# Kernel optimization log

Measured on AMD Instinct MI355X. Metric: run time of the kernel, lower is better.

The kernel has to match this reference:

```python
import math
import jax, jax.numpy as jnp
import numpy as np

B, L, D = 8, 512, 32
SEQ_LEN = 512.0
N_PATCHES, N_REF = 16, 32
LAT, HM = 128, 4
FH, NL, FF = 8, 3, 128
PRED = 96

def _time_embed(t, d):
    # interleaved sin/cos embedding, matching PositionalEmbedding's div_term
    div = jnp.exp(jnp.arange(0, d, 2, dtype=jnp.float32) * (-math.log(10000.0) / d))
    ang = t[..., None] * div
    out = jnp.zeros(t.shape + (d,), dtype=jnp.float32)
    return out.at[..., 0::2].set(jnp.sin(ang)).at[..., 1::2].set(jnp.cos(ang))

def _layernorm(x, g, b):
    mu = jnp.mean(x, axis=-1, keepdims=True)
    var = jnp.var(x, axis=-1, keepdims=True)
    return (x - mu) / jnp.sqrt(var + 1e-5) * g + b

def _mha(z, Wq, Wk, Wv, Wo, bq, bk, bv, bo):
    N, S, dm = z.shape
    hd = dm // FH
    q = (z @ Wq + bq).reshape(N, S, FH, hd)
    k = (z @ Wk + bk).reshape(N, S, FH, hd)
    v = (z @ Wv + bv).reshape(N, S, FH, hd)
    s = jnp.einsum('nqhe,nkhe->nhqk', q, k) / math.sqrt(hd)
    a = jax.nn.softmax(s, axis=-1)
    o = jnp.einsum('nhqk,nkhe->nqhe', a, v).reshape(N, S, dm)
    return o @ Wo + bo

def _forward(x, x_mark, x_mask, Wq, Wk, W_out, b_out, f_Wq, f_Wk, f_Wv, f_Wo, f_bq, f_bk, f_bv, f_bo, f_ln1_g, f_ln1_b, f_W1, f_b1, f_W2, f_b2, f_ln2_g, f_ln2_b, ln_f_g, ln_f_b, W_lin, b_lin):
    t = x_mark[:, :, 0]                                   # [B, L] irregular timestamps in [0, SEQ_LEN]
    edges = jnp.linspace(0.0, SEQ_LEN, N_PATCHES + 1)
    refs = jnp.linspace(0.0, SEQ_LEN, N_REF * N_PATCHES).reshape(N_PATCHES, N_REF)
    obs_valid = jnp.sum(x_mask, axis=-1) > 0              # [B, L]
    dk = LAT // HM
    Kmat = (_time_embed(t, LAT) @ Wk).reshape(B, L, HM, dk)
    v = x * x_mask                                        # mask values like `v = v * m` in original
    reprs = []
    for i in range(N_PATCHES):  # fixed small structural loop
        # _split_patch equivalent: per-channel masked attention is permutation
        # invariant, so the sort/scatter compaction reduces to masking.
        in_patch = (t >= edges[i]) & (t <= edges[i + 1]) & obs_valid   # [B, L]
        Qi = (_time_embed(refs[i], LAT) @ Wq).reshape(N_REF, HM, dk)
        scores = jnp.einsum('rhe,blhe->bhrl', Qi, Kmat) / math.sqrt(dk)
        cmask = x_mask * in_patch[..., None].astype(x.dtype)           # [B, L, D]
        neg = jnp.where(cmask[:, None, None, :, :] > 0, 0.0, -1e9)     # [B,1,1,L,D]
        p = jax.nn.softmax(scores[..., None] + neg, axis=3)            # [B,H,R,L,D]
        attn = jnp.einsum('bhrld,bld->brhd', p, v)                     # [B,R,H,D]
        reprs.append(attn.reshape(B, N_REF, HM * D) @ W_out + b_out)   # [B,R,D]
    rp = jnp.stack(reprs, axis=1)                          # [B, NP, R, D]
    z = rp.transpose(0, 3, 1, 2).reshape(B * D, N_PATCHES, N_REF)
    z = z + _time_embed(jnp.arange(N_PATCHES, dtype=jnp.float32), N_REF)[None]
    for l in range(NL):
        a = _mha(z, f_Wq[l], f_Wk[l], f_Wv[l], f_Wo[l], f_bq[l], f_bk[l], f_bv[l], f_bo[l])
        z = _layernorm(z + a, f_ln1_g[l], f_ln1_b[l])
        y = jax.nn.gelu(z @ f_W1[l] + f_b1[l]) @ f_W2[l] + f_b2[l]
        z = _layernorm(z + y, f_ln2_g[l], f_ln2_b[l])
    z = _layernorm(z, ln_f_g, ln_f_b)
    emb = z.reshape(B, D, N_PATCHES, N_REF).transpose(0, 1, 3, 2)      # [B, D, R, NP]
    out = emb.reshape(B, D, N_REF * N_PATCHES) @ W_lin + b_lin         # [B, D, PRED]
    return out.transpose(0, 2, 1)                          # [B, PRED, D]

def setup_inputs():
    key = jax.random.key(0)
    ks = jax.random.split(key, 30)
    def w(i, shape, fan_in):
        return jax.random.normal(ks[i], shape, jnp.float32) / math.sqrt(fan_in)
    return {
        'x': jax.random.normal(ks[0], (B, L, D), jnp.float32),
        'x_mark': jnp.sort(jax.random.uniform(ks[1], (B, L, 1), jnp.float32) * SEQ_LEN, axis=1),
        'x_mask': (jax.random.uniform(ks[2], (B, L, D), jnp.float32) < 0.8).astype(jnp.float32),
        'Wq': w(3, (LAT, LAT), LAT),
        'Wk': w(4, (LAT, LAT), LAT),
        'W_out': w(5, (HM * D, D), HM * D),
        'b_out': jnp.zeros((D,), jnp.float32),
        'f_Wq': w(6, (NL, N_REF, N_REF), N_REF),
        'f_Wk': w(7, (NL, N_REF, N_REF), N_REF),
        'f_Wv': w(8, (NL, N_REF, N_REF), N_REF),
        'f_Wo': w(9, (NL, N_REF, N_REF), N_REF),
        'f_bq': jnp.zeros((NL, N_REF), jnp.float32),
        'f_bk': jnp.zeros((NL, N_REF), jnp.float32),
        'f_bv': jnp.zeros((NL, N_REF), jnp.float32),
        'f_bo': jnp.zeros((NL, N_REF), jnp.float32),
        'f_ln1_g': jnp.ones((NL, N_REF), jnp.float32),
        'f_ln1_b': jnp.zeros((NL, N_REF), jnp.float32),
        'f_W1': w(10, (NL, N_REF, FF), N_REF),
        'f_b1': jnp.zeros((NL, FF), jnp.float32),
        'f_W2': w(11, (NL, FF, N_REF), FF),
        'f_b2': jnp.zeros((NL, N_REF), jnp.float32),
        'f_ln2_g': jnp.ones((NL, N_REF), jnp.float32),
        'f_ln2_b': jnp.zeros((NL, N_REF), jnp.float32),
        'ln_f_g': jnp.ones((N_REF,), jnp.float32),
        'ln_f_b': jnp.zeros((N_REF,), jnp.float32),
        'W_lin': w(12, (N_REF * N_PATCHES, PRED), N_REF * N_PATCHES),
        'b_lin': jnp.zeros((PRED,), jnp.float32),
    }

def reference(x, x_mark, x_mask, Wq, Wk, W_out, b_out, f_Wq, f_Wk, f_Wv, f_Wo, f_bq, f_bk, f_bv, f_bo, f_ln1_g, f_ln1_b, f_W1, f_b1, f_W2, f_b2, f_ln2_g, f_ln2_b, ln_f_g, ln_f_b, W_lin, b_lin):
    return _forward(x, x_mark, x_mask, Wq, Wk, W_out, b_out, f_Wq, f_Wk, f_Wv, f_Wo, f_bq, f_bk, f_bv, f_bo, f_ln1_g, f_ln1_b, f_W1, f_b1, f_W2, f_b2, f_ln2_g, f_ln2_b, ln_f_g, ln_f_b, W_lin, b_lin)
```

## Files before the change

kernel.cpp:

```cpp
#include <hip/hip_runtime.h>
#include <math.h>


#define ISQ32 0.17677669529663687f
#define C128  (-0.07195578415606394f)
#define C32   (-0.28782313662425575f)

__launch_bounds__(256)
__global__ void k_embed_mm(const float* __restrict__ x_mark,
                           const float* __restrict__ Wk,
                           const float* __restrict__ Wq,
                           const float* __restrict__ x_mask,
                           float* __restrict__ Kmat,
                           float* __restrict__ Qall,
                           unsigned* __restrict__ obsBits) {
    if (blockIdx.x >= 144) {
        const int gt = (blockIdx.x - 144) * 256 + threadIdx.x;
        const int w = gt >> 6, lane = gt & 63;
        const int bl = w * 2 + (lane >> 5);
        const int d = lane & 31;
        const unsigned long long mm = __ballot(x_mask[bl * 32 + d] > 0.0f);
        if (lane == 0)  obsBits[w * 2]     = (unsigned)(mm & 0xffffffffull);
        if (lane == 32) obsBits[w * 2 + 1] = (unsigned)(mm >> 32);
        return;
    }
    __shared__ float sTe[32][128];
    const int wv = threadIdx.x >> 6;
    const int lane = threadIdx.x & 63;
    const int bb = blockIdx.x;
    const int row0 = bb * 32 + wv * 8;
    const float dv = __expf((float)(2 * lane) * C128);
    #pragma unroll
    for (int rr = 0; rr < 8; ++rr) {
        const int row = row0 + rr;
        const float t = (row < 4096) ? x_mark[row] : (float)(row - 4096) * (512.0f / 511.0f);
        const float ang = t * dv;
        sTe[wv * 8 + rr][2 * lane]     = __sinf(ang);
        sTe[wv * 8 + rr][2 * lane + 1] = __cosf(ang);
    }
    __syncthreads();
    const float* W = (bb < 128) ? Wk : Wq;
    float a0[8], a1[8];
    #pragma unroll
    for (int rr = 0; rr < 8; ++rr) { a0[rr] = 0.f; a1[rr] = 0.f; }
    for (int k = 0; k < 128; ++k) {
        const float wa = W[k * 128 + lane];
        const float wb = W[k * 128 + lane + 64];
        #pragma unroll
        for (int rr = 0; rr < 8; ++rr) {
            const float te = sTe[wv * 8 + rr][k];
            a0[rr] = fmaf(te, wa, a0[rr]);
            a1[rr] = fmaf(te, wb, a1[rr]);
        }
    }
    #pragma unroll
    for (int rr = 0; rr < 8; ++rr) {
        const int row = row0 + rr;
        float* outp = (row < 4096) ? (Kmat + row * 128) : (Qall + (row - 4096) * 128);
        outp[lane] = a0[rr];
        outp[lane + 64] = a1[rr];
    }
}

__launch_bounds__(256)
__global__ void k_patch_attn(const float* __restrict__ x,
                             const float* __restrict__ x_mark,
                             const unsigned* __restrict__ obsBits,
                             const float* __restrict__ Kmat,
                             const float* __restrict__ Qall,
                             float* __restrict__ attn) {
    __shared__ float sQ[32][36];
    __shared__ float sK[96][36];
    __shared__ float sX[96][36];
    __shared__ float sS[32][100];
    __shared__ unsigned sBits[96];
    __shared__ int sLo, sHi;
    __shared__ unsigned sAV;
    const int tid = threadIdx.x;
    const int h = blockIdx.x & 3;
    const int b = (blockIdx.x >> 2) & 7;
    const int i = blockIdx.x >> 5;
    const float e0 = 32.0f * (float)i, e1 = 32.0f * (float)(i + 1);
    if (tid == 0) { sLo = 512; sHi = -1; sAV = 0u; }
    __syncthreads();
    #pragma unroll
    for (int k = 0; k < 4; ++k) {
        const int idx = tid + 256 * k;
        sQ[idx >> 5][idx & 31] = Qall[(i * 32 + (idx >> 5)) * 128 + h * 32 + (idx & 31)];
    }
    {
        int mylo = 512, myhi = -1;
        unsigned mybits = 0u;
        #pragma unroll
        for (int k = 0; k < 2; ++k) {
            const int l = tid + 256 * k;
            const float t = x_mark[b * 512 + l];
            if (t >= e0 && t <= e1) {
                mylo = min(mylo, l);
                myhi = max(myhi, l);
                mybits |= obsBits[b * 512 + l];
            }
        }
        #pragma unroll
        for (int off = 32; off > 0; off >>= 1) {
            mylo = min(mylo, __shfl_xor(mylo, off));
            myhi = max(myhi, __shfl_xor(myhi, off));
            mybits |= __shfl_xor(mybits, off);
        }
        if ((tid & 63) == 0) {
            atomicMin(&sLo, mylo);
            atomicMax(&sHi, myhi);
            atomicOr(&sAV, mybits);
        }
    }
    __syncthreads();
    const int lo = sLo, hi = sHi;
    const int NA = hi - lo + 1;
    const unsigned av = sAV;
    const int r = tid >> 3, dg = tid & 7;

    if (NA >= 1 && NA <= 96 && av == 0xffffffffu) {
        if (tid < NA) sBits[tid] = obsBits[b * 512 + lo + tid];
        for (int idx = tid; idx < NA * 32; idx += 256) {
            const int ll = idx >> 5, c = idx & 31;
            sK[ll][c] = Kmat[(b * 512 + lo + ll) * 128 + h * 32 + c];
            sX[ll][c] = x[(b * 512 + lo + ll) * 32 + c];
        }
        __syncthreads();
        float m = -1e30f;
        for (int ll = dg; ll < NA; ll += 8) {
            float p0 = 0.f, p1 = 0.f, p2 = 0.f, p3 = 0.f;
            #pragma unroll
            for (int e = 0; e < 32; e += 4) {
                p0 = fmaf(sQ[r][e],     sK[ll][e],     p0);
                p1 = fmaf(sQ[r][e + 1], sK[ll][e + 1], p1);
                p2 = fmaf(sQ[r][e + 2], sK[ll][e + 2], p2);
                p3 = fmaf(sQ[r][e + 3], sK[ll][e + 3], p3);
            }
            const float s = (p0 + p1 + p2 + p3) * ISQ32;
            sS[r][ll] = s;
            m = fmaxf(m, s);
        }
        #pragma unroll
        for (int off = 4; off > 0; off >>= 1) m = fmaxf(m, __shfl_xor(m, off));
        for (int ll = dg; ll < NA; ll += 8) sS[r][ll] = __expf(sS[r][ll] - m);
        __syncthreads();
        float num0 = 0.f, num1 = 0.f, num2 = 0.f, num3 = 0.f;
        float den0 = 0.f, den1 = 0.f, den2 = 0.f, den3 = 0.f;
        for (int ll = 0; ll < NA; ++ll) {
            const float e = sS[r][ll];
            const unsigned bits = sBits[ll];
            if ((bits >> dg) & 1u)        { den0 += e; num0 = fmaf(e, sX[ll][dg],      num0); }
            if ((bits >> (dg + 8)) & 1u)  { den1 += e; num1 = fmaf(e, sX[ll][dg + 8],  num1); }
            if ((bits >> (dg + 16)) & 1u) { den2 += e; num2 = fmaf(e, sX[ll][dg + 16], num2); }
            if ((bits >> (dg + 24)) & 1u) { den3 += e; num3 = fmaf(e, sX[ll][dg + 24], num3); }
        }
        float* ap = attn + ((i * 8 + b) * 32 + r) * 128 + h * 32;
        ap[dg]      = num0 / den0;
        ap[dg + 8]  = num1 / den1;
        ap[dg + 16] = num2 / den2;
        ap[dg + 24] = num3 / den3;
    } else {
        float m = -1e30f;
        float num[4] = {0.f, 0.f, 0.f, 0.f}, den[4] = {0.f, 0.f, 0.f, 0.f};
        for (int l = 0; l < 512; ++l) {
            const float t = x_mark[b * 512 + l];
            const unsigned bits = obsBits[b * 512 + l];
            const bool inr = (t >= e0 && t <= e1);
            const unsigned effD = (inr ? bits : 0u) | ~av;
            if (effD == 0u) continue;
            const unsigned effN = effD & bits;
            const float* Kp = Kmat + (b * 512 + l) * 128 + h * 32;
            float a = 0.f;
            #pragma unroll
            for (int e2 = 0; e2 < 32; ++e2) a = fmaf(sQ[r][e2], Kp[e2], a);
            const float s = a * ISQ32;
            float eNew;
            if (s > m) {
                const float scale = __expf(m - s);
                #pragma unroll
                for (int jj = 0; jj < 4; ++jj) { den[jj] *= scale; num[jj] *= scale; }
                m = s;
                eNew = 1.0f;
            } else {
                eNew = __expf(s - m);
            }
            const float* xp = x + (b * 512 + l) * 32;
            #pragma unroll
            for (int jj = 0; jj < 4; ++jj) {
                const int d = dg + 8 * jj;
                if ((effD >> d) & 1u) den[jj] += eNew;
                if ((effN >> d) & 1u) num[jj] = fmaf(eNew, xp[d], num[jj]);
            }
        }
        float* ap = attn + ((i * 8 + b) * 32 + r) * 128 + h * 32;
        #pragma unroll
        for (int jj = 0; jj < 4; ++jj) ap[dg + 8 * jj] = num[jj] / den[jj];
    }
}

__global__ void k_reprs(const float* __restrict__ attn,
                        const float* __restrict__ W_out,
                        const float* __restrict__ b_out,
                        float* __restrict__ z) {
    __shared__ float sA[32][129];
    const int tid = threadIdx.x;
    const int b = blockIdx.x & 7;
    const int i = blockIdx.x >> 3;
    #pragma unroll
    for (int k = 0; k < 16; ++k) {
        const int idx = tid + 256 * k;
        sA[idx >> 7][idx & 127] = attn[(i * 8 + b) * 4096 + idx];
    }
    __syncthreads();
    const int r = tid & 31, dgrp = tid >> 5;
    float acc0 = 0.f, acc1 = 0.f, acc2 = 0.f, acc3 = 0.f;
    #pragma unroll 8
    for (int k = 0; k < 128; ++k) {
        const float a = sA[r][k];
        acc0 = fmaf(a, W_out[k * 32 + dgrp],      acc0);
        acc1 = fmaf(a, W_out[k * 32 + dgrp + 8],  acc1);
        acc2 = fmaf(a, W_out[k * 32 + dgrp + 16], acc2);
        acc3 = fmaf(a, W_out[k * 32 + dgrp + 24], acc3);
    }
    const float dv = expf((float)(2 * (r >> 1)) * C32);
    const float ang = (float)i * dv;
    const float pe = (r & 1) ? cosf(ang) : sinf(ang);
    const int base = i * 32 + r;
    z[(b * 32 + dgrp)      * 512 + base] = acc0 + b_out[dgrp]      + pe;
    z[(b * 32 + dgrp + 8)  * 512 + base] = acc1 + b_out[dgrp + 8]  + pe;
    z[(b * 32 + dgrp + 16) * 512 + base] = acc2 + b_out[dgrp + 16] + pe;
    z[(b * 32 + dgrp + 24) * 512 + base] = acc3 + b_out[dgrp + 24] + pe;
}

#define QKV6(ax, bx, kk) { \
    const float wq_ = sWq[(kk) * 32 + j]; \
    const float wk_ = sWk[(kk) * 32 + j]; \
    const float wv_ = sWv[(kk) * 32 + j]; \
    qa = fmaf(ax, wq_, qa); qb = fmaf(bx, wq_, qb); \
    ka = fmaf(ax, wk_, ka); kb = fmaf(bx, wk_, kb); \
    va = fmaf(ax, wv_, va); vb = fmaf(bx, wv_, vb); }
#define OP2(ax, bx, kk) { \
    const float w_ = sWo[(kk) * 32 + j]; \
    oa = fmaf(ax, w_, oa); ob = fmaf(bx, w_, ob); }
#define F2(ax, bx, kk) { \
    const float w_ = sW2[(kk) * 32 + j]; \
    fa = fmaf(ax, w_, fa); fb = fmaf(bx, w_, fb); }

__launch_bounds__(256, 1)
__global__ void k_former(const float* __restrict__ z,
                         const float* __restrict__ f_Wq, const float* __restrict__ f_Wk,
                         const float* __restrict__ f_Wv, const float* __restrict__ f_Wo,
                         const float* __restrict__ f_bq, const float* __restrict__ f_bk,
                         const float* __restrict__ f_bv, const float* __restrict__ f_bo,
                         const float* __restrict__ f_ln1_g, const float* __restrict__ f_ln1_b,
                         const float* __restrict__ f_W1, const float* __restrict__ f_b1,
                         const float* __restrict__ f_W2, const float* __restrict__ f_b2,
                         const float* __restrict__ f_ln2_g, const float* __restrict__ f_ln2_b,
                         const float* __restrict__ ln_f_g, const float* __restrict__ ln_f_b,
                         const float* __restrict__ W_lin, const float* __restrict__ b_lin,
                         float* __restrict__ out) {
    __shared__ float sWq[1024], sWk[1024], sWv[1024], sWo[1024];
    __shared__ float sW1[4096], sW2[4096];
    __shared__ float sZ[16][32];
    __shared__ float sQs[16][33], sKs[16][33], sVs[16][33];
    __shared__ float sO[16][32];
    __shared__ float sH[16][128];
    __shared__ float sZf[512];
    __shared__ float sPart[2][96];
    const int tid = threadIdx.x;
    const int n = blockIdx.x;
    const int j = tid & 31, s2 = tid >> 5;
    const int sA = s2 * 2, sB = sA + 1;
    const int g = tid >> 6, t64 = tid & 63;
    const float* Wg = (g == 0) ? f_Wq : ((g == 1) ? f_Wk : ((g == 2) ? f_Wv : f_Wo));
    float* dstg = (g == 0) ? sWq : ((g == 1) ? sWk : ((g == 2) ? sWv : sWo));

    #pragma unroll
    for (int k = 0; k < 2; ++k) {
        const int idx = tid + 256 * k;
        sZ[idx >> 5][idx & 31] = z[n * 512 + idx];
    }
    float zlocA = z[n * 512 + sA * 32 + j];
    float zlocB = z[n * 512 + sB * 32 + j];
    {
        float4 rq[4], r1[4], r2[4];
        #pragma unroll
        for (int rep = 0; rep < 4; ++rep) rq[rep] = ((const float4*)Wg)[rep * 64 + t64];
        #pragma unroll
        for (int rep = 0; rep < 4; ++rep) r1[rep] = ((const float4*)f_W1)[rep * 256 + tid];
        #pragma unroll
        for (int rep = 0; rep < 4; ++rep) r2[rep] = ((const float4*)f_W2)[rep * 256 + tid];
        #pragma unroll
        for (int rep = 0; rep < 4; ++rep) ((float4*)dstg)[rep * 64 + t64] = rq[rep];
        #pragma unroll
        for (int rep = 0; rep < 4; ++rep) ((float4*)sW1)[rep * 256 + tid] = r1[rep];
        #pragma unroll
        for (int rep = 0; rep < 4; ++rep) ((float4*)sW2)[rep * 256 + tid] = r2[rep];
    }
    __syncthreads();

    float4 nq[4], n1[4], n2[4];
    for (int layer = 0; layer < 3; ++layer) {
        if (layer < 2) {
            const int offQ = (layer + 1) * 1024, offF = (layer + 1) * 4096;
            #pragma unroll
            for (int rep = 0; rep < 4; ++rep) nq[rep] = ((const float4*)(Wg + offQ))[rep * 64 + t64];
            #pragma unroll
            for (int rep = 0; rep < 4; ++rep) n1[rep] = ((const float4*)(f_W1 + offF))[rep * 256 + tid];
            #pragma unroll
            for (int rep = 0; rep < 4; ++rep) n2[rep] = ((const float4*)(f_W2 + offF))[rep * 256 + tid];
        }
        {
            const float bq = f_bq[layer * 32 + j], bk = f_bk[layer * 32 + j], bv = f_bv[layer * 32 + j];
            float qa = 0.f, qb = 0.f, ka = 0.f, kb = 0.f, va = 0.f, vb = 0.f;
            const float4* zra = (const float4*)&sZ[sA][0];
            const float4* zrb = (const float4*)&sZ[sB][0];
            #pragma unroll
            for (int k4 = 0; k4 < 8; ++k4) {
                const float4 a = zra[k4], b4 = zrb[k4];
                QKV6(a.x, b4.x, 4 * k4 + 0)
                QKV6(a.y, b4.y, 4 * k4 + 1)
                QKV6(a.z, b4.z, 4 * k4 + 2)
                QKV6(a.w, b4.w, 4 * k4 + 3)
            }
            sQs[sA][j] = qa + bq; sQs[sB][j] = qb + bq;
            sKs[sA][j] = ka + bk; sKs[sB][j] = kb + bk;
            sVs[sA][j] = va + bv; sVs[sB][j] = vb + bv;
        }
        __syncthreads();
        {
            const int q = tid & 15, hh = (tid >> 4) & 7, half = tid >> 7;
            float sc[16];
            float mx = -1e30f;
            #pragma unroll
            for (int k = 0; k < 16; ++k) {
                float a = 0.f;
                #pragma unroll
                for (int e = 0; e < 4; ++e) a = fmaf(sQs[q][hh * 4 + e], sKs[k][hh * 4 + e], a);
                sc[k] = a * 0.5f;
                mx = fmaxf(mx, sc[k]);
            }
            float sum = 0.f;
            #pragma unroll
            for (int k = 0; k < 16; ++k) { sc[k] = __expf(sc[k] - mx); sum += sc[k]; }
            const float inv = 1.0f / sum;
            #pragma unroll
            for (int m = 0; m < 2; ++m) {
                const int e = half * 2 + m;
                float a = 0.f;
                #pragma unroll
                for (int k = 0; k < 16; ++k) a = fmaf(sc[k], sVs[k][hh * 4 + e], a);
                sO[q][hh * 4 + e] = a * inv;
            }
        }
        __syncthreads();
        {
            const float bo = f_bo[layer * 32 + j];
            const float g1 = f_ln1_g[layer * 32 + j], be1 = f_ln1_b[layer * 32 + j];
            float oa = 0.f, ob = 0.f;
            const float4* ora = (const float4*)&sO[sA][0];
            const float4* orb = (const float4*)&sO[sB][0];
            #pragma unroll
            for (int k4 = 0; k4 < 8; ++k4) {
                const float4 a = ora[k4], b4 = orb[k4];
                OP2(a.x, b4.x, 4 * k4 + 0)
                OP2(a.y, b4.y, 4 * k4 + 1)
                OP2(a.z, b4.z, 4 * k4 + 2)
                OP2(a.w, b4.w, 4 * k4 + 3)
            }
            const float tA = zlocA + oa + bo, tB = zlocB + ob + bo;
            float sumA = tA, sqA = tA * tA, sumB = tB, sqB = tB * tB;
            #pragma unroll
            for (int off = 16; off > 0; off >>= 1) {
                sumA += __shfl_xor(sumA, off); sqA += __shfl_xor(sqA, off);
                sumB += __shfl_xor(sumB, off); sqB += __shfl_xor(sqB, off);
            }
            const float muA = sumA * (1.0f / 32.0f);
            const float rsA = rsqrtf(sqA * (1.0f / 32.0f) - muA * muA + 1e-5f);
            const float muB = sumB * (1.0f / 32.0f);
            const float rsB = rsqrtf(sqB * (1.0f / 32.0f) - muB * muB + 1e-5f);
            zlocA = (tA - muA) * rsA * g1 + be1;
            zlocB = (tB - muB) * rsB * g1 + be1;
            sZ[sA][j] = zlocA;
            sZ[sB][j] = zlocB;
        }
        __syncthreads();
        {
            const int f = tid & 127, sh = tid >> 7;
            const float b1v = f_b1[layer * 128 + f];
            float w1c[32];
            #pragma unroll
            for (int k = 0; k < 32; ++k) w1c[k] = sW1[k * 128 + f];
            #pragma unroll
            for (int ss = 0; ss < 8; ++ss) {
                const int s = sh * 8 + ss;
                const float4* zr = (const float4*)&sZ[s][0];
                float acc = b1v;
                #pragma unroll
                for (int k4 = 0; k4 < 8; ++k4) {
                    const float4 a = zr[k4];
                    acc = fmaf(a.x, w1c[4 * k4], acc);     acc = fmaf(a.y, w1c[4 * k4 + 1], acc);
                    acc = fmaf(a.z, w1c[4 * k4 + 2], acc); acc = fmaf(a.w, w1c[4 * k4 + 3], acc);
                }
                const float c = acc;
                const float a2 = 1.5957691216057308f * (c + 0.044715f * c * c * c);
                const float e = __expf(a2);
                sH[s][f] = 0.5f * c * (2.0f - 2.0f / (e + 1.0f));
            }
        }
        __syncthreads();
        {
            const float b2v = f_b2[layer * 32 + j];
            const float g2 = f_ln2_g[layer * 32 + j], be2 = f_ln2_b[layer * 32 + j];
            float fa = 0.f, fb = 0.f;
            const float4* hra = (const float4*)&sH[sA][0];
            const float4* hrb = (const float4*)&sH[sB][0];
            #pragma unroll
            for (int k4 = 0; k4 < 32; ++k4) {
                const float4 a = hra[k4], b4 = hrb[k4];
                F2(a.x, b4.x, 4 * k4 + 0)
                F2(a.y, b4.y, 4 * k4 + 1)
                F2(a.z, b4.z, 4 * k4 + 2)
                F2(a.w, b4.w, 4 * k4 + 3)
            }
            const float tA = zlocA + fa + b2v, tB = zlocB + fb + b2v;
            float sumA = tA, sqA = tA * tA, sumB = tB, sqB = tB * tB;
            #pragma unroll
            for (int off = 16; off > 0; off >>= 1) {
                sumA += __shfl_xor(sumA, off); sqA += __shfl_xor(sqA, off);
                sumB += __shfl_xor(sumB, off); sqB += __shfl_xor(sqB, off);
            }
            const float muA = sumA * (1.0f / 32.0f);
            const float rsA = rsqrtf(sqA * (1.0f / 32.0f) - muA * muA + 1e-5f);
            const float muB = sumB * (1.0f / 32.0f);
            const float rsB = rsqrtf(sqB * (1.0f / 32.0f) - muB * muB + 1e-5f);
            zlocA = (tA - muA) * rsA * g2 + be2;
            zlocB = (tB - muB) * rsB * g2 + be2;
            sZ[sA][j] = zlocA;
            sZ[sB][j] = zlocB;
        }
        __syncthreads();
        if (layer < 2) {
            #pragma unroll
            for (int rep = 0; rep < 4; ++rep) ((float4*)dstg)[rep * 64 + t64] = nq[rep];
            #pragma unroll
            for (int rep = 0; rep < 4; ++rep) ((float4*)sW1)[rep * 256 + tid] = n1[rep];
            #pragma unroll
            for (int rep = 0; rep < 4; ++rep) ((float4*)sW2)[rep * 256 + tid] = n2[rep];
            __syncthreads();
        }
    }
    {
        float sumA = zlocA, sqA = zlocA * zlocA, sumB = zlocB, sqB = zlocB * zlocB;
        #pragma unroll
        for (int off = 16; off > 0; off >>= 1) {
            sumA += __shfl_xor(sumA, off); sqA += __shfl_xor(sqA, off);
            sumB += __shfl_xor(sumB, off); sqB += __shfl_xor(sqB, off);
        }
        const float muA = sumA * (1.0f / 32.0f);
        const float rsA = rsqrtf(sqA * (1.0f / 32.0f) - muA * muA + 1e-5f);
        const float muB = sumB * (1.0f / 32.0f);
        const float rsB = rsqrtf(sqB * (1.0f / 32.0f) - muB * muB + 1e-5f);
        const float gf = ln_f_g[j], bf = ln_f_b[j];
        sZf[j * 16 + sA] = (zlocA - muA) * rsA * gf + bf;
        sZf[j * 16 + sB] = (zlocB - muB) * rsB * gf + bf;
    }
    __syncthreads();
    if (tid < 192) {
        const int half = tid / 96, o = tid % 96;
        const int j0 = half * 256;
        float acc = 0.f;
        #pragma unroll 16
        for (int jj = 0; jj < 256; ++jj)
            acc = fmaf(sZf[j0 + jj], W_lin[(j0 + jj) * 96 + o], acc);
        sPart[half][o] = acc;
    }
    __syncthreads();
    if (tid < 96)
        out[((n >> 5) * 96 + tid) * 32 + (n & 31)] = sPart[0][tid] + sPart[1][tid] + b_lin[tid];
}

extern "C" void kernel_launch(void* const* d_in, const int* in_sizes, int n_in,
                              void* d_out, int out_size, void* d_ws, size_t ws_size,
                              hipStream_t stream) {
    const float* x       = (const float*)d_in[0];
    const float* x_mark  = (const float*)d_in[1];
    const float* x_mask  = (const float*)d_in[2];
    const float* Wq      = (const float*)d_in[3];
    const float* Wk      = (const float*)d_in[4];
    const float* W_out   = (const float*)d_in[5];
    const float* b_out   = (const float*)d_in[6];
    const float* f_Wq    = (const float*)d_in[7];
    const float* f_Wk    = (const float*)d_in[8];
    const float* f_Wv    = (const float*)d_in[9];
    const float* f_Wo    = (const float*)d_in[10];
    const float* f_bq    = (const float*)d_in[11];
    const float* f_bk    = (const float*)d_in[12];
    const float* f_bv    = (const float*)d_in[13];
    const float* f_bo    = (const float*)d_in[14];
    const float* f_ln1_g = (const float*)d_in[15];
    const float* f_ln1_b = (const float*)d_in[16];
    const float* f_W1    = (const float*)d_in[17];
    const float* f_b1    = (const float*)d_in[18];
    const float* f_W2    = (const float*)d_in[19];
    const float* f_b2    = (const float*)d_in[20];
    const float* f_ln2_g = (const float*)d_in[21];
    const float* f_ln2_b = (const float*)d_in[22];
    const float* ln_f_g  = (const float*)d_in[23];
    const float* ln_f_b  = (const float*)d_in[24];
    const float* W_lin   = (const float*)d_in[25];
    const float* b_lin   = (const float*)d_in[26];

    float* ws = (float*)d_ws;
    float* Kmat      = ws;
    float* Qall      = ws + 524288;
    unsigned* obsB   = (unsigned*)(ws + 589824);
    float* attn      = ws + 593920;
    float* zbuf      = ws + 1118208;

    k_embed_mm<<<656, 256, 0, stream>>>(x_mark, Wk, Wq, x_mask, Kmat, Qall, obsB);
    k_patch_attn<<<512, 256, 0, stream>>>(x, x_mark, obsB, Kmat, Qall, attn);
    k_reprs<<<128, 256, 0, stream>>>(attn, W_out, b_out, zbuf);
    k_former<<<256, 256, 0, stream>>>(zbuf,
        f_Wq, f_Wk, f_Wv, f_Wo, f_bq, f_bk, f_bv, f_bo,
        f_ln1_g, f_ln1_b, f_W1, f_b1, f_W2, f_b2, f_ln2_g, f_ln2_b,
        ln_f_g, ln_f_b, W_lin, b_lin, (float*)d_out);
}
```

Before: 72.83 us.

## Restructure former kernel so each wavefront owns whole sequence rows, cutting block barriers

Rewrites the per-layer transformer block so each 16-lane group in a wavefront owns one sequence position and computes two output columns. Attention, the output projection, the FFN and both layernorms then exchange data only through wave shuffles and same-wave shared rows, which removes most __syncthreads per layer. W1 is stored transposed with padding for conflict-free reads. The final linear is spread across all threads with a shared-memory reduction. In exchange, weight staging for the next layer is now synchronous between layers instead of prefetched into registers, and the head uses a 16-lane split of the softmax.

```diff
diff --git a/kernel.cpp b/kernel.cpp
--- a/kernel.cpp
+++ b/kernel.cpp
@@ -233,20 +233,6 @@
     z[(b * 32 + dgrp + 24) * 512 + base] = acc3 + b_out[dgrp + 24] + pe;
 }
 
-#define QKV6(ax, bx, kk) { \
-    const float wq_ = sWq[(kk) * 32 + j]; \
-    const float wk_ = sWk[(kk) * 32 + j]; \
-    const float wv_ = sWv[(kk) * 32 + j]; \
-    qa = fmaf(ax, wq_, qa); qb = fmaf(bx, wq_, qb); \
-    ka = fmaf(ax, wk_, ka); kb = fmaf(bx, wk_, kb); \
-    va = fmaf(ax, wv_, va); vb = fmaf(bx, wv_, vb); }
-#define OP2(ax, bx, kk) { \
-    const float w_ = sWo[(kk) * 32 + j]; \
-    oa = fmaf(ax, w_, oa); ob = fmaf(bx, w_, ob); }
-#define F2(ax, bx, kk) { \
-    const float w_ = sW2[(kk) * 32 + j]; \
-    fa = fmaf(ax, w_, fa); fb = fmaf(bx, w_, fb); }
-
 __launch_bounds__(256, 1)
 __global__ void k_former(const float* __restrict__ z,
                          const float* __restrict__ f_Wq, const float* __restrict__ f_Wk,
@@ -260,148 +246,151 @@
                          const float* __restrict__ ln_f_g, const float* __restrict__ ln_f_b,
                          const float* __restrict__ W_lin, const float* __restrict__ b_lin,
                          float* __restrict__ out) {
-    __shared__ float sWq[1024], sWk[1024], sWv[1024], sWo[1024];
-    __shared__ float sW1[4096], sW2[4096];
-    __shared__ float sZ[16][32];
-    __shared__ float sQs[16][33], sKs[16][33], sVs[16][33];
-    __shared__ float sO[16][32];
-    __shared__ float sH[16][128];
-    __shared__ float sZf[512];
-    __shared__ float sPart[2][96];
+    __shared__ float wbuf[12800];
+    __shared__ float sKmat[16][36], sVmat[16][36];
+    __shared__ float sZrow[16][36], sOrow[16][36];
+    __shared__ float sH[16][132];
     const int tid = threadIdx.x;
     const int n = blockIdx.x;
-    const int j = tid & 31, s2 = tid >> 5;
-    const int sA = s2 * 2, sB = sA + 1;
-    const int g = tid >> 6, t64 = tid & 63;
-    const float* Wg = (g == 0) ? f_Wq : ((g == 1) ? f_Wk : ((g == 2) ? f_Wv : f_Wo));
-    float* dstg = (g == 0) ? sWq : ((g == 1) ? sWk : ((g == 2) ? sWv : sWo));
-
-    #pragma unroll
-    for (int k = 0; k < 2; ++k) {
-        const int idx = tid + 256 * k;
-        sZ[idx >> 5][idx & 31] = z[n * 512 + idx];
-    }
-    float zlocA = z[n * 512 + sA * 32 + j];
-    float zlocB = z[n * 512 + sB * 32 + j];
+    const int lane64 = tid & 63;
+    const int w = tid >> 6;
+    const int sLoc = lane64 >> 4;
+    const int s = w * 4 + sLoc;
+    const int l16 = lane64 & 15;
+    const int j0 = 2 * l16;
+    const int gbase = lane64 & 48;
+
+    #define STAGE_LAYER(l) { \
+        ((float4*)wbuf)[tid]       = ((const float4*)(f_Wq + (l) * 1024))[tid]; \
+        ((float4*)wbuf)[256 + tid] = ((const float4*)(f_Wk + (l) * 1024))[tid]; \
+        ((float4*)wbuf)[512 + tid] = ((const float4*)(f_Wv + (l) * 1024))[tid]; \
+        ((float4*)wbuf)[768 + tid] = ((const float4*)(f_Wo + (l) * 1024))[tid]; \
+        _Pragma("unroll") \
+        for (int r2 = 0; r2 < 4; ++r2) { \
+            const int idx4 = r2 * 256 + tid; \
+            const int kk = idx4 >> 5, f4 = (idx4 & 31) << 2; \
+            const float4 v = ((const float4*)(f_W1 + (l) * 4096))[idx4]; \
+            wbuf[4096 + (f4 + 0) * 36 + kk] = v.x; \
+            wbuf[4096 + (f4 + 1) * 36 + kk] = v.y; \
+            wbuf[4096 + (f4 + 2) * 36 + kk] = v.z; \
+            wbuf[4096 + (f4 + 3) * 36 + kk] = v.w; \
+        } \
+        _Pragma("unroll") \
+        for (int r2 = 0; r2 < 4; ++r2) \
+            ((float4*)(wbuf + 8704))[r2 * 256 + tid] = ((const float4*)(f_W2 + (l) * 4096))[r2 * 256 + tid]; \
+    }
+
     {
-        float4 rq[4], r1[4], r2[4];
-        #pragma unroll
-        for (int rep = 0; rep < 4; ++rep) rq[rep] = ((const float4*)Wg)[rep * 64 + t64];
-        #pragma unroll
-        for (int rep = 0; rep < 4; ++rep) r1[rep] = ((const float4*)f_W1)[rep * 256 + tid];
-        #pragma unroll
-        for (int rep = 0; rep < 4; ++rep) r2[rep] = ((const float4*)f_W2)[rep * 256 + tid];
-        #pragma unroll
-        for (int rep = 0; rep < 4; ++rep) ((float4*)dstg)[rep * 64 + t64] = rq[rep];
-        #pragma unroll
-        for (int rep = 0; rep < 4; ++rep) ((float4*)sW1)[rep * 256 + tid] = r1[rep];
-        #pragma unroll
-        for (int rep = 0; rep < 4; ++rep) ((float4*)sW2)[rep * 256 + tid] = r2[rep];
-    }
+        const int ps = tid >> 4, pj = (tid & 15) * 2;
+        *(float2*)&sZrow[ps][pj] = *(const float2*)(z + n * 512 + ps * 32 + pj);
+    }
+    STAGE_LAYER(0)
     __syncthreads();
 
-    float4 nq[4], n1[4], n2[4];
-    for (int layer = 0; layer < 3; ++layer) {
-        if (layer < 2) {
-            const int offQ = (layer + 1) * 1024, offF = (layer + 1) * 4096;
-            #pragma unroll
-            for (int rep = 0; rep < 4; ++rep) nq[rep] = ((const float4*)(Wg + offQ))[rep * 64 + t64];
-            #pragma unroll
-            for (int rep = 0; rep < 4; ++rep) n1[rep] = ((const float4*)(f_W1 + offF))[rep * 256 + tid];
-            #pragma unroll
-            for (int rep = 0; rep < 4; ++rep) n2[rep] = ((const float4*)(f_W2 + offF))[rep * 256 + tid];
-        }
+    for (int l = 0; l < 3; ++l) {
+        float q0, q1;
         {
-            const float bq = f_bq[layer * 32 + j], bk = f_bk[layer * 32 + j], bv = f_bv[layer * 32 + j];
+            float4 zr[8];
+            #pragma unroll
+            for (int k4 = 0; k4 < 8; ++k4) zr[k4] = *(const float4*)&sZrow[s][4 * k4];
+            const float2 bq = *(const float2*)(f_bq + l * 32 + j0);
+            const float2 bk = *(const float2*)(f_bk + l * 32 + j0);
+            const float2 bv = *(const float2*)(f_bv + l * 32 + j0);
             float qa = 0.f, qb = 0.f, ka = 0.f, kb = 0.f, va = 0.f, vb = 0.f;
-            const float4* zra = (const float4*)&sZ[sA][0];
-            const float4* zrb = (const float4*)&sZ[sB][0];
             #pragma unroll
             for (int k4 = 0; k4 < 8; ++k4) {
-                const float4 a = zra[k4], b4 = zrb[k4];
-                QKV6(a.x, b4.x, 4 * k4 + 0)
-                QKV6(a.y, b4.y, 4 * k4 + 1)
-                QKV6(a.z, b4.z, 4 * k4 + 2)
-                QKV6(a.w, b4.w, 4 * k4 + 3)
-            }
-            sQs[sA][j] = qa + bq; sQs[sB][j] = qb + bq;
-            sKs[sA][j] = ka + bk; sKs[sB][j] = kb + bk;
-            sVs[sA][j] = va + bv; sVs[sB][j] = vb + bv;
+                #pragma unroll
+                for (int e = 0; e < 4; ++e) {
+                    const int kk = 4 * k4 + e;
+                    const float zz = (e == 0) ? zr[k4].x : (e == 1) ? zr[k4].y : (e == 2) ? zr[k4].z : zr[k4].w;
+                    const float2 wq = *(const float2*)&wbuf[kk * 32 + j0];
+                    const float2 wk2 = *(const float2*)&wbuf[1024 + kk * 32 + j0];
+                    const float2 wv2 = *(const float2*)&wbuf[2048 + kk * 32 + j0];
+                    qa = fmaf(zz, wq.x, qa);  qb = fmaf(zz, wq.y, qb);
+                    ka = fmaf(zz, wk2.x, ka); kb = fmaf(zz, wk2.y, kb);
+                    va = fmaf(zz, wv2.x, va); vb = fmaf(zz, wv2.y, vb);
+                }
+            }
+            q0 = qa + bq.x; q1 = qb + bq.y;
+            *(float2*)&sKmat[s][j0] = make_float2(ka + bk.x, kb + bk.y);
+            *(float2*)&sVmat[s][j0] = make_float2(va + bv.x, vb + bv.y);
         }
         __syncthreads();
         {
-            const int q = tid & 15, hh = (tid >> 4) & 7, half = tid >> 7;
-            float sc[16];
-            float mx = -1e30f;
-            #pragma unroll
-            for (int k = 0; k < 16; ++k) {
-                float a = 0.f;
+            const int hh = l16 & 7, kh = l16 >> 3;
+            const int h4 = hh * 4;
+            const float qa = __shfl(q0, gbase + 2 * hh);
+            const float qb = __shfl(q1, gbase + 2 * hh);
+            const float qc = __shfl(q0, gbase + 2 * hh + 1);
+            const float qd = __shfl(q1, gbase + 2 * hh + 1);
+            float sc[8];
+            #pragma unroll
+            for (int m = 0; m < 8; ++m) {
+                const int kk = kh * 8 + m;
+                const float4 kv = *(const float4*)&sKmat[kk][h4];
+                sc[m] = (qa * kv.x + qb * kv.y + qc * kv.z + qd * kv.w) * 0.5f;
+            }
+            float mx = sc[0];
+            #pragma unroll
+            for (int m = 1; m < 8; ++m) mx = fmaxf(mx, sc[m]);
+            mx = fmaxf(mx, __shfl_xor(mx, 8));
+            float sum = 0.f;
+            #pragma unroll
+            for (int m = 0; m < 8; ++m) { sc[m] = __expf(sc[m] - mx); sum += sc[m]; }
+            sum += __shfl_xor(sum, 8);
+            const float inv = 1.0f / sum;
+            float o0 = 0.f, o1 = 0.f, o2 = 0.f, o3 = 0.f;
+            #pragma unroll
+            for (int m = 0; m < 8; ++m) {
+                const int kk = kh * 8 + m;
+                const float4 vv = *(const float4*)&sVmat[kk][h4];
+                o0 = fmaf(sc[m], vv.x, o0); o1 = fmaf(sc[m], vv.y, o1);
+                o2 = fmaf(sc[m], vv.z, o2); o3 = fmaf(sc[m], vv.w, o3);
+            }
+            o0 += __shfl_xor(o0, 8); o1 += __shfl_xor(o1, 8);
+            o2 += __shfl_xor(o2, 8); o3 += __shfl_xor(o3, 8);
+            if (kh == 0)
+                *(float4*)&sOrow[s][h4] = make_float4(o0 * inv, o1 * inv, o2 * inv, o3 * inv);
+        }
+        {
+            float oacc0 = 0.f, oacc1 = 0.f;
+            #pragma unroll
+            for (int k4 = 0; k4 < 8; ++k4) {
+                const float4 ov = *(const float4*)&sOrow[s][4 * k4];
                 #pragma unroll
-                for (int e = 0; e < 4; ++e) a = fmaf(sQs[q][hh * 4 + e], sKs[k][hh * 4 + e], a);
-                sc[k] = a * 0.5f;
-                mx = fmaxf(mx, sc[k]);
-            }
-            float sum = 0.f;
-            #pragma unroll
-            for (int k = 0; k < 16; ++k) { sc[k] = __expf(sc[k] - mx); sum += sc[k]; }
-            const float inv = 1.0f / sum;
-            #pragma unroll
-            for (int m = 0; m < 2; ++m) {
-                const int e = half * 2 + m;
-                float a = 0.f;
-                #pragma unroll
-                for (int k = 0; k < 16; ++k) a = fmaf(sc[k], sVs[k][hh * 4 + e], a);
-                sO[q][hh * 4 + e] = a * inv;
-            }
-        }
-        __syncthreads();
+                for (int e = 0; e < 4; ++e) {
+                    const float oe = (e == 0) ? ov.x : (e == 1) ? ov.y : (e == 2) ? ov.z : ov.w;
+                    const float2 wo = *(const float2*)&wbuf[3072 + (4 * k4 + e) * 32 + j0];
+                    oacc0 = fmaf(oe, wo.x, oacc0); oacc1 = fmaf(oe, wo.y, oacc1);
+                }
+            }
+            const float2 bo = *(const float2*)(f_bo + l * 32 + j0);
+            const float2 zold = *(const float2*)&sZrow[s][j0];
+            const float t0 = zold.x + oacc0 + bo.x;
+            const float t1 = zold.y + oacc1 + bo.y;
+            float sm = t0 + t1, sq = t0 * t0 + t1 * t1;
+            #pragma unroll
+            for (int off = 8; off > 0; off >>= 1) { sm += __shfl_xor(sm, off); sq += __shfl_xor(sq, off); }
+            const float mu = sm * (1.0f / 32.0f);
+            const float rs = rsqrtf(sq * (1.0f / 32.0f) - mu * mu + 1e-5f);
+            const float2 g1 = *(const float2*)(f_ln1_g + l * 32 + j0);
+            const float2 be1 = *(const float2*)(f_ln1_b + l * 32 + j0);
+            *(float2*)&sZrow[s][j0] = make_float2((t0 - mu) * rs * g1.x + be1.x,
+                                                  (t1 - mu) * rs * g1.y + be1.y);
+        }
         {
-            const float bo = f_bo[layer * 32 + j];
-            const float g1 = f_ln1_g[layer * 32 + j], be1 = f_ln1_b[layer * 32 + j];
-            float oa = 0.f, ob = 0.f;
-            const float4* ora = (const float4*)&sO[sA][0];
-            const float4* orb = (const float4*)&sO[sB][0];
-            #pragma unroll
-            for (int k4 = 0; k4 < 8; ++k4) {
-                const float4 a = ora[k4], b4 = orb[k4];
-                OP2(a.x, b4.x, 4 * k4 + 0)
-                OP2(a.y, b4.y, 4 * k4 + 1)
-                OP2(a.z, b4.z, 4 * k4 + 2)
-                OP2(a.w, b4.w, 4 * k4 + 3)
-            }
-            const float tA = zlocA + oa + bo, tB = zlocB + ob + bo;
-            float sumA = tA, sqA = tA * tA, sumB = tB, sqB = tB * tB;
-            #pragma unroll
-            for (int off = 16; off > 0; off >>= 1) {
-                sumA += __shfl_xor(sumA, off); sqA += __shfl_xor(sqA, off);
-                sumB += __shfl_xor(sumB, off); sqB += __shfl_xor(sqB, off);
-            }
-            const float muA = sumA * (1.0f / 32.0f);
-            const float rsA = rsqrtf(sqA * (1.0f / 32.0f) - muA * muA + 1e-5f);
-            const float muB = sumB * (1.0f / 32.0f);
-            const float rsB = rsqrtf(sqB * (1.0f / 32.0f) - muB * muB + 1e-5f);
-            zlocA = (tA - muA) * rsA * g1 + be1;
-            zlocB = (tB - muB) * rsB * g1 + be1;
-            sZ[sA][j] = zlocA;
-            sZ[sB][j] = zlocB;
-        }
-        __syncthreads();
-        {
-            const int f = tid & 127, sh = tid >> 7;
-            const float b1v = f_b1[layer * 128 + f];
-            float w1c[32];
-            #pragma unroll
-            for (int k = 0; k < 32; ++k) w1c[k] = sW1[k * 128 + f];
-            #pragma unroll
-            for (int ss = 0; ss < 8; ++ss) {
-                const int s = sh * 8 + ss;
-                const float4* zr = (const float4*)&sZ[s][0];
-                float acc = b1v;
+            float4 zr[8];
+            #pragma unroll
+            for (int k4 = 0; k4 < 8; ++k4) zr[k4] = *(const float4*)&sZrow[s][4 * k4];
+            #pragma unroll
+            for (int m = 0; m < 8; ++m) {
+                const int f = l16 + 16 * m;
+                float acc = f_b1[l * 128 + f];
                 #pragma unroll
                 for (int k4 = 0; k4 < 8; ++k4) {
-                    const float4 a = zr[k4];
-                    acc = fmaf(a.x, w1c[4 * k4], acc);     acc = fmaf(a.y, w1c[4 * k4 + 1], acc);
-                    acc = fmaf(a.z, w1c[4 * k4 + 2], acc); acc = fmaf(a.w, w1c[4 * k4 + 3], acc);
+                    const float4 w14 = *(const float4*)&wbuf[4096 + f * 36 + 4 * k4];
+                    acc = fmaf(zr[k4].x, w14.x, acc); acc = fmaf(zr[k4].y, w14.y, acc);
+                    acc = fmaf(zr[k4].z, w14.z, acc); acc = fmaf(zr[k4].w, w14.w, acc);
                 }
                 const float c = acc;
                 const float a2 = 1.5957691216057308f * (c + 0.044715f * c * c * c);
@@ -409,76 +398,85 @@
                 sH[s][f] = 0.5f * c * (2.0f - 2.0f / (e + 1.0f));
             }
         }
-        __syncthreads();
         {
-            const float b2v = f_b2[layer * 32 + j];
-            const float g2 = f_ln2_g[layer * 32 + j], be2 = f_ln2_b[layer * 32 + j];
+            const float2 b2v = *(const float2*)(f_b2 + l * 32 + j0);
             float fa = 0.f, fb = 0.f;
-            const float4* hra = (const float4*)&sH[sA][0];
-            const float4* hrb = (const float4*)&sH[sB][0];
-            #pragma unroll
-            for (int k4 = 0; k4 < 32; ++k4) {
-                const float4 a = hra[k4], b4 = hrb[k4];
-                F2(a.x, b4.x, 4 * k4 + 0)
-                F2(a.y, b4.y, 4 * k4 + 1)
-                F2(a.z, b4.z, 4 * k4 + 2)
-                F2(a.w, b4.w, 4 * k4 + 3)
-            }
-            const float tA = zlocA + fa + b2v, tB = zlocB + fb + b2v;
-            float sumA = tA, sqA = tA * tA, sumB = tB, sqB = tB * tB;
-            #pragma unroll
-            for (int off = 16; off > 0; off >>= 1) {
-                sumA += __shfl_xor(sumA, off); sqA += __shfl_xor(sqA, off);
-                sumB += __shfl_xor(sumB, off); sqB += __shfl_xor(sqB, off);
-            }
-            const float muA = sumA * (1.0f / 32.0f);
-            const float rsA = rsqrtf(sqA * (1.0f / 32.0f) - muA * muA + 1e-5f);
-            const float muB = sumB * (1.0f / 32.0f);
-            const float rsB = rsqrtf(sqB * (1.0f / 32.0f) - muB * muB + 1e-5f);
-            zlocA = (tA - muA) * rsA * g2 + be2;
-            zlocB = (tB - muB) * rsB * g2 + be2;
-            sZ[sA][j] = zlocA;
-            sZ[sB][j] = zlocB;
-        }
-        __syncthreads();
-        if (layer < 2) {
-            #pragma unroll
-            for (int rep = 0; rep < 4; ++rep) ((float4*)dstg)[rep * 64 + t64] = nq[rep];
-            #pragma unroll
-            for (int rep = 0; rep < 4; ++rep) ((float4*)sW1)[rep * 256 + tid] = n1[rep];
-            #pragma unroll
-            for (int rep = 0; rep < 4; ++rep) ((float4*)sW2)[rep * 256 + tid] = n2[rep];
+            #pragma unroll
+            for (int f4 = 0; f4 < 32; ++f4) {
+                const float4 hv = *(const float4*)&sH[s][4 * f4];
+                #pragma unroll
+                for (int e = 0; e < 4; ++e) {
+                    const float he = (e == 0) ? hv.x : (e == 1) ? hv.y : (e == 2) ? hv.z : hv.w;
+                    const float2 w2 = *(const float2*)&wbuf[8704 + (4 * f4 + e) * 32 + j0];
+                    fa = fmaf(he, w2.x, fa); fb = fmaf(he, w2.y, fb);
+                }
+            }
+            const float2 zold = *(const float2*)&sZrow[s][j0];
+            const float t0 = zold.x + fa + b2v.x;
+            const float t1 = zold.y + fb + b2v.y;
+            float sm = t0 + t1, sq = t0 * t0 + t1 * t1;
+            #pragma unroll
+            for (int off = 8; off > 0; off >>= 1) { sm += __shfl_xor(sm, off); sq += __shfl_xor(sq, off); }
+            const float mu = sm * (1.0f / 32.0f);
+            const float rs = rsqrtf(sq * (1.0f / 32.0f) - mu * mu + 1e-5f);
+            const float2 g2 = *(const float2*)(f_ln2_g + l * 32 + j0);
+            const float2 be2 = *(const float2*)(f_ln2_b + l * 32 + j0);
+            *(float2*)&sZrow[s][j0] = make_float2((t0 - mu) * rs * g2.x + be2.x,
+                                                  (t1 - mu) * rs * g2.y + be2.y);
+        }
+        if (l < 2) {
             __syncthreads();
+            if (l == 0) STAGE_LAYER(1) else STAGE_LAYER(2)
+            __syncthreads();
         }
     }
     {
-        float sumA = zlocA, sqA = zlocA * zlocA, sumB = zlocB, sqB = zlocB * zlocB;
-        #pragma unroll
-        for (int off = 16; off > 0; off >>= 1) {
-            sumA += __shfl_xor(sumA, off); sqA += __shfl_xor(sqA, off);
-            sumB += __shfl_xor(sumB, off); sqB += __shfl_xor(sqB, off);
-        }
-        const float muA = sumA * (1.0f / 32.0f);
-        const float rsA = rsqrtf(sqA * (1.0f / 32.0f) - muA * muA + 1e-5f);
-        const float muB = sumB * (1.0f / 32.0f);
-        const float rsB = rsqrtf(sqB * (1.0f / 32.0f) - muB * muB + 1e-5f);
-        const float gf = ln_f_g[j], bf = ln_f_b[j];
-        sZf[j * 16 + sA] = (zlocA - muA) * rsA * gf + bf;
-        sZf[j * 16 + sB] = (zlocB - muB) * rsB * gf + bf;
+        const float2 zv = *(const float2*)&sZrow[s][j0];
+        const float t0 = zv.x, t1 = zv.y;
+        float sm = t0 + t1, sq = t0 * t0 + t1 * t1;
+        #pragma unroll
+        for (int off = 8; off > 0; off >>= 1) { sm += __shfl_xor(sm, off); sq += __shfl_xor(sq, off); }
+        const float mu = sm * (1.0f / 32.0f);
+        const float rs = rsqrtf(sq * (1.0f / 32.0f) - mu * mu + 1e-5f);
+        const float2 gf = *(const float2*)(ln_f_g + j0);
+        const float2 bf = *(const float2*)(ln_f_b + j0);
+        *(float2*)&sZrow[s][j0] = make_float2((t0 - mu) * rs * gf.x + bf.x,
+                                              (t1 - mu) * rs * gf.y + bf.y);
+    }
+    {
+        float* sRed = &sH[0][0];
+        float4 zr[8];
+        #pragma unroll
+        for (int k4 = 0; k4 < 8; ++k4) zr[k4] = *(const float4*)&sZrow[s][4 * k4];
+        const int o0 = 6 * l16;
+        float p0 = 0.f, p1 = 0.f, p2 = 0.f, p3 = 0.f, p4 = 0.f, p5 = 0.f;
+        #pragma unroll
+        for (int k4 = 0; k4 < 8; ++k4) {
+            #pragma unroll
+            for (int e = 0; e < 4; ++e) {
+                const int rr = 4 * k4 + e;
+                const float zz = (e == 0) ? zr[k4].x : (e == 1) ? zr[k4].y : (e == 2) ? zr[k4].z : zr[k4].w;
+                const float* wl = W_lin + (rr * 16 + s) * 96 + o0;
+                const float2 wa = *(const float2*)(wl);
+                const float2 wb = *(const float2*)(wl + 2);
+                const float2 wc = *(const float2*)(wl + 4);
+                p0 = fmaf(zz, wa.x, p0); p1 = fmaf(zz, wa.y, p1);
+                p2 = fmaf(zz, wb.x, p2); p3 = fmaf(zz, wb.y, p3);
+                p4 = fmaf(zz, wc.x, p4); p5 = fmaf(zz, wc.y, p5);
+            }
+        }
+        *(float2*)&sRed[s * 100 + o0]     = make_float2(p0, p1);
+        *(float2*)&sRed[s * 100 + o0 + 2] = make_float2(p2, p3);
+        *(float2*)&sRed[s * 100 + o0 + 4] = make_float2(p4, p5);
     }
     __syncthreads();
-    if (tid < 192) {
-        const int half = tid / 96, o = tid % 96;
-        const int j0 = half * 256;
-        float acc = 0.f;
-        #pragma unroll 16
-        for (int jj = 0; jj < 256; ++jj)
-            acc = fmaf(sZf[j0 + jj], W_lin[(j0 + jj) * 96 + o], acc);
-        sPart[half][o] = acc;
-    }
-    __syncthreads();
-    if (tid < 96)
-        out[((n >> 5) * 96 + tid) * 32 + (n & 31)] = sPart[0][tid] + sPart[1][tid] + b_lin[tid];
+    if (tid < 96) {
+        const float* sRed = &sH[0][0];
+        float acc = b_lin[tid];
+        #pragma unroll
+        for (int ss = 0; ss < 16; ++ss) acc += sRed[ss * 100 + tid];
+        out[((n >> 5) * 96 + tid) * 32 + (n & 31)] = acc;
+    }
 }
 
 extern "C" void kernel_launch(void* const* d_in, const int* in_sizes, int n_in,
```

Result: faster. 62.70 us (-13.9%).
